# Performance work log

Hardware: AMD Instinct MI355X
Metric: run time of the kernel (lower is better)

## Reference

```python
import jax, jax.numpy as jnp
import numpy as np

TEMPERATURE = 0.1
B, D = 8192, 128
NUM_CLASSES = 100

def setup_inputs() -> dict:
    key = jax.random.key(0)
    k1, k2 = jax.random.split(key)
    embeddings = jax.random.normal(k1, (B, D), dtype=jnp.float32)
    labels = jax.random.randint(k2, (B,), 0, NUM_CLASSES, dtype=jnp.int64)
    return {"embeddings": embeddings, "labels": labels}

def reference(embeddings, labels):
    b = embeddings.shape[0]
    # L2-normalize rows (F.normalize with eps to avoid div-by-zero)
    norm = jnp.maximum(jnp.linalg.norm(embeddings, axis=1, keepdims=True), 1e-12)
    emb = embeddings / norm
    # [B, B] cosine similarities scaled by temperature
    sim = jnp.matmul(emb, emb.T) / TEMPERATURE
    eye = jnp.eye(b, dtype=jnp.float32)
    pos_mask = (labels[:, None] == labels[None, :]).astype(jnp.float32) - eye
    all_mask = 1.0 - eye
    # Original computes exp(sim*mask)*mask; since mask is {0,1}, this equals
    # exp(sim) summed over the masked entries.
    exp_sim = jnp.exp(sim)
    pos_sum = jnp.sum(exp_sim * pos_mask, axis=1)  # sum over positives j != i
    all_sum = jnp.sum(exp_sim * all_mask, axis=1)  # sum over all j != i
    valid = pos_sum > 0.0  # rows with no positives are skipped in the original
    pos_safe = jnp.where(valid, pos_sum, 1.0)
    all_safe = jnp.where(valid, all_sum, 1.0)
    row_loss = -jnp.log(pos_safe / all_safe)
    n_valid = jnp.sum(valid.astype(jnp.float32))
    loss = jnp.sum(jnp.where(valid, row_loss, 0.0)) / jnp.maximum(n_valid, 1.0)
    return loss
```

## Files before the change

kernel.cpp:

```cpp
#include <hip/hip_runtime.h>
#include <hip/hip_bf16.h>


#define B_ROWS 8192
#define D_DIM 128
#define K_SCALE 14.426950408889634f
#define JSPLIT 32
#define JCHUNK (B_ROWS / JSPLIT)
#define TILE_J 64
#define NT (JCHUNK / TILE_J)
#define BM 256

typedef __attribute__((ext_vector_type(8))) short bf16x8;
typedef __attribute__((ext_vector_type(16))) float f32x16;
typedef __attribute__((ext_vector_type(4))) unsigned int u32x4;
typedef unsigned int u32;
typedef unsigned long long u64;

static __device__ __forceinline__ unsigned short bf16_bits(float x) {
  __hip_bfloat16 h = __float2bfloat16(x);
  unsigned short u;
  __builtin_memcpy(&u, &h, 2);
  return u;
}
static __device__ __forceinline__ float f32_from_bits(u32 b) {
  float f;
  __builtin_memcpy(&f, &b, 4);
  return f;
}
static __device__ __forceinline__ float bf16f(unsigned short u) {
  return f32_from_bits((u32)u << 16);
}

__global__ __launch_bounds__(256) void prep_kernel(
    const float* __restrict__ E, const long long* __restrict__ labels,
    __hip_bfloat16* __restrict__ Ebf, __hip_bfloat16* __restrict__ Ebf2,
    int* __restrict__ lab32, unsigned char* __restrict__ lab8p,
    float* __restrict__ diag, u32* __restrict__ ticket) {
  if (blockIdx.x == 0 && threadIdx.x == 0) *ticket = 0u;
  const int wid = threadIdx.x >> 6, lane = threadIdx.x & 63;
  const int row = blockIdx.x * 4 + wid;
  const float2 v = *(const float2*)(E + (u64)row * D_DIM + lane * 2);
  float ss = v.x * v.x + v.y * v.y;
#pragma unroll
  for (int m = 1; m < 64; m <<= 1) ss += __shfl_xor(ss, m);
  const float scale = 1.0f / fmaxf(sqrtf(ss), 1e-12f);
  const unsigned short bx = bf16_bits(v.x * scale);
  const unsigned short by = bf16_bits(v.y * scale);
  ((u32*)Ebf)[(u64)row * (D_DIM / 2) + lane] = ((u32)by << 16) | bx;
  const float fx = bf16f(bx), fy = bf16f(by);
  const unsigned short axb = bf16_bits(fx * K_SCALE);
  const unsigned short ayb = bf16_bits(fy * K_SCALE);
  ((u32*)Ebf2)[(u64)row * (D_DIM / 2) + lane] = ((u32)ayb << 16) | axb;
  float dot = bf16f(axb) * fx + bf16f(ayb) * fy;
#pragma unroll
  for (int m = 1; m < 64; m <<= 1) dot += __shfl_xor(dot, m);
  if (lane == 0) diag[row] = __builtin_amdgcn_exp2f(dot);

  const int gtid = blockIdx.x * 256 + threadIdx.x;
  if (gtid < B_ROWS) {
    const int lab = (int)labels[gtid];
    lab32[gtid] = lab;
    const int local = gtid & 31;
    const int h = (local >> 2) & 1;
    const int r = (local & 3) + 4 * (local >> 3);
    lab8p[(gtid & ~31) + h * 16 + r] = (unsigned char)lab;
  }
}

__global__ __launch_bounds__(256, 3) void sim_kernel(
    const __hip_bfloat16* __restrict__ Ebf,
    const __hip_bfloat16* __restrict__ Ebf2, const int* __restrict__ lab32,
    const unsigned char* __restrict__ lab8p, float* __restrict__ pos_part,
    float* __restrict__ all_part) {
  __shared__ __align__(16) unsigned char lds[2][TILE_J * 256];

  const int t = threadIdx.x;
  const int wid = t >> 6, lane = t & 63;
  const int l31 = lane & 31, hi = lane >> 5;
  const int i0w = blockIdx.x * BM + wid * 64;
  const int jbase0 = blockIdx.y * JCHUNK;

  bf16x8 ifragA[8], ifragB[8];
  {
    const __hip_bfloat16* srcA = Ebf2 + (u64)(i0w + l31) * D_DIM + hi * 8;
    const __hip_bfloat16* srcB = srcA + 32 * D_DIM;
#pragma unroll
    for (int ks = 0; ks < 8; ++ks) {
      ifragA[ks] = *(const bf16x8*)(srcA + ks * 16);
      ifragB[ks] = *(const bf16x8*)(srcB + ks * 16);
    }
  }
  const int labi0 = lab32[i0w + l31];
  const int labi1 = lab32[i0w + 32 + l31];

  const u32 key = lane & 15;
  const u32 M = (key & 14) << 4;
  const u32 base2 = (u32)(l31 * 256) + (((hi ^ (key & 1)) & 1) << 4);

  const unsigned char* gsrc[4];
  {
    const unsigned char* gb = (const unsigned char*)Ebf;
    const int l4 = lane >> 4, sl = lane & 15;
#pragma unroll
    for (int i = 0; i < 4; ++i) {
      const int rloc = wid * 16 + i * 4 + l4;
      gsrc[i] =
          gb + (u64)(jbase0 + rloc) * 256 + (u64)((sl ^ (i * 4 + l4)) * 16);
    }
  }

  auto stage = [&](int buf) {
#pragma unroll
    for (int i = 0; i < 4; ++i) {
      __builtin_amdgcn_global_load_lds(
          (const __attribute__((address_space(1))) u32*)(gsrc[i]),
          (__attribute__((address_space(3)))
               u32*)(&lds[buf][wid * 4096 + i * 1024]),
          16, 0, 0);
      gsrc[i] += TILE_J * 256;
    }
  };

  float pos0 = 0.f, pos1 = 0.f, all0 = 0.f, all1 = 0.f;

  stage(0);
  __syncthreads();

  for (int tile = 0; tile < NT; ++tile) {
    const int cur = tile & 1;
    if (tile + 1 < NT) stage(cur ^ 1);
    const int jbase = jbase0 + tile * TILE_J;
    const unsigned char* lbuf = lds[cur];
#pragma unroll
    for (int jsub = 0; jsub < 2; ++jsub) {
      f32x16 acc0 = {}, acc1 = {};
#pragma unroll
      for (int ks = 0; ks < 8; ++ks) {
        bf16x8 jfrag = *(const bf16x8*)(lbuf + base2 +
                                        (((u32)(ks << 5)) ^ M) + jsub * 8192);
        acc0 = __builtin_amdgcn_mfma_f32_32x32x16_bf16(jfrag, ifragA[ks], acc0,
                                                       0, 0, 0);
        acc1 = __builtin_amdgcn_mfma_f32_32x32x16_bf16(jfrag, ifragB[ks], acc1,
                                                       0, 0, 0);
      }
      const u32x4 labv = *(const u32x4*)(lab8p + jbase + jsub * 32 + hi * 16);
#pragma unroll
      for (int r = 0; r < 16; ++r) {
        const int labj = (int)((labv[r >> 2] >> ((r & 3) * 8)) & 0xff);
        const float p0 = __builtin_amdgcn_exp2f(acc0[r]);
        const float p1 = __builtin_amdgcn_exp2f(acc1[r]);
        all0 += p0;
        all1 += p1;
        pos0 += (labj == labi0) ? p0 : 0.f;
        pos1 += (labj == labi1) ? p1 : 0.f;
      }
    }
    __syncthreads();
  }

  pos0 += __shfl_xor(pos0, 32);
  all0 += __shfl_xor(all0, 32);
  pos1 += __shfl_xor(pos1, 32);
  all1 += __shfl_xor(all1, 32);
  if (hi == 0) {
    const u64 off = (u64)blockIdx.y * B_ROWS;
    pos_part[off + i0w + l31] = pos0;
    all_part[off + i0w + l31] = all0;
    pos_part[off + i0w + 32 + l31] = pos1;
    all_part[off + i0w + 32 + l31] = all1;
  }
}

__global__ __launch_bounds__(256) void fin_kernel(
    const float* __restrict__ pos_part, const float* __restrict__ all_part,
    const float* __restrict__ diag, float* __restrict__ fin_s,
    float* __restrict__ fin_c, u32* __restrict__ ticket,
    float* __restrict__ out) {
  const int row = blockIdx.x * 256 + threadIdx.x;
  float ps = 0.f, as_ = 0.f;
#pragma unroll
  for (int js = 0; js < JSPLIT; ++js) {
    ps += pos_part[(u64)js * B_ROWS + row];
    as_ += all_part[(u64)js * B_ROWS + row];
  }
  const float d = diag[row];
  ps -= d;
  as_ -= d;
  float s = 0.f, c = 0.f;
  if (ps > 0.f) {
    s = logf(as_) - logf(ps);
    c = 1.f;
  }
#pragma unroll
  for (int m = 1; m < 64; m <<= 1) {
    s += __shfl_xor(s, m);
    c += __shfl_xor(c, m);
  }
  __shared__ float ls[4], lc[4];
  const int wid = threadIdx.x >> 6, lane = threadIdx.x & 63;
  if (lane == 0) {
    ls[wid] = s;
    lc[wid] = c;
  }
  __syncthreads();
  if (threadIdx.x == 0) {
    __hip_atomic_store(&fin_s[blockIdx.x], ls[0] + ls[1] + ls[2] + ls[3],
                       __ATOMIC_RELEASE, __HIP_MEMORY_SCOPE_AGENT);
    __hip_atomic_store(&fin_c[blockIdx.x], lc[0] + lc[1] + lc[2] + lc[3],
                       __ATOMIC_RELEASE, __HIP_MEMORY_SCOPE_AGENT);
    const u32 tk = __hip_atomic_fetch_add(ticket, 1u, __ATOMIC_ACQ_REL,
                                          __HIP_MEMORY_SCOPE_AGENT);
    if (tk == 31u) {
      float ts = 0.f, tc = 0.f;
      for (int b = 0; b < 32; ++b) {
        ts += __hip_atomic_load(&fin_s[b], __ATOMIC_ACQUIRE,
                                __HIP_MEMORY_SCOPE_AGENT);
        tc += __hip_atomic_load(&fin_c[b], __ATOMIC_ACQUIRE,
                                __HIP_MEMORY_SCOPE_AGENT);
      }
      out[0] = ts / fmaxf(tc, 1.0f);
    }
  }
}

extern "C" void kernel_launch(void* const* d_in, const int* in_sizes, int n_in,
                              void* d_out, int out_size, void* d_ws,
                              size_t ws_size, hipStream_t stream) {
  const float* E = (const float*)d_in[0];
  const long long* labels = (const long long*)d_in[1];

  float* pos_part = (float*)d_ws;
  float* all_part = pos_part + JSPLIT * B_ROWS;
  int* lab32 = (int*)(all_part + JSPLIT * B_ROWS);
  float* diag = (float*)(lab32 + B_ROWS);
  unsigned char* lab8p = (unsigned char*)(diag + B_ROWS);
  float* fin_s = (float*)(lab8p + B_ROWS);
  float* fin_c = fin_s + 32;
  u32* ticket = (u32*)(fin_c + 32);
  __hip_bfloat16* Ebf = (__hip_bfloat16*)(ticket + 4);
  __hip_bfloat16* Ebf2 = Ebf + (u64)B_ROWS * D_DIM;

  prep_kernel<<<B_ROWS / 4, 256, 0, stream>>>(E, labels, Ebf, Ebf2, lab32,
                                              lab8p, diag, ticket);
  sim_kernel<<<dim3(B_ROWS / BM, JSPLIT), 256, 0, stream>>>(
      Ebf, Ebf2, lab32, lab8p, pos_part, all_part);
  fin_kernel<<<JSPLIT, 256, 0, stream>>>(pos_part, all_part, diag, fin_s,
                                         fin_c, ticket, (float*)d_out);
}
```

Before: 53.28 us.

## Drop LDS staging in sim kernel, load j-fragments directly from global memory

The sim kernel no longer stages j-tiles into double-buffered LDS with global_load_lds and barriers. Each wave now loads its bf16 j-fragments straight from global memory (L2-cached) into registers before the MFMAs. JSPLIT doubles to 64 so each block handles 128 j rows, which gives twice as many blocks and removes the occupancy hint. This cuts LDS traffic and syncs, but every wave re-reads the same j data from cache, and the fin kernel now has to reduce twice as many partials.

```diff
diff --git a/kernel.cpp b/kernel.cpp
--- a/kernel.cpp
+++ b/kernel.cpp
@@ -5,10 +5,9 @@
 #define B_ROWS 8192
 #define D_DIM 128
 #define K_SCALE 14.426950408889634f
-#define JSPLIT 32
+#define JSPLIT 64
 #define JCHUNK (B_ROWS / JSPLIT)
-#define TILE_J 64
-#define NT (JCHUNK / TILE_J)
+#define NSUB (JCHUNK / 32)
 #define BM 256
 
 typedef __attribute__((ext_vector_type(8))) short bf16x8;
@@ -68,13 +67,11 @@
   }
 }
 
-__global__ __launch_bounds__(256, 3) void sim_kernel(
+__global__ __launch_bounds__(256) void sim_kernel(
     const __hip_bfloat16* __restrict__ Ebf,
     const __hip_bfloat16* __restrict__ Ebf2, const int* __restrict__ lab32,
     const unsigned char* __restrict__ lab8p, float* __restrict__ pos_part,
     float* __restrict__ all_part) {
-  __shared__ __align__(16) unsigned char lds[2][TILE_J * 256];
-
   const int t = threadIdx.x;
   const int wid = t >> 6, lane = t & 63;
   const int l31 = lane & 31, hi = lane >> 5;
@@ -94,69 +91,39 @@
   const int labi0 = lab32[i0w + l31];
   const int labi1 = lab32[i0w + 32 + l31];
 
-  const u32 key = lane & 15;
-  const u32 M = (key & 14) << 4;
-  const u32 base2 = (u32)(l31 * 256) + (((hi ^ (key & 1)) & 1) << 4);
-
-  const unsigned char* gsrc[4];
-  {
-    const unsigned char* gb = (const unsigned char*)Ebf;
-    const int l4 = lane >> 4, sl = lane & 15;
-#pragma unroll
-    for (int i = 0; i < 4; ++i) {
-      const int rloc = wid * 16 + i * 4 + l4;
-      gsrc[i] =
-          gb + (u64)(jbase0 + rloc) * 256 + (u64)((sl ^ (i * 4 + l4)) * 16);
-    }
-  }
-
-  auto stage = [&](int buf) {
-#pragma unroll
-    for (int i = 0; i < 4; ++i) {
-      __builtin_amdgcn_global_load_lds(
-          (const __attribute__((address_space(1))) u32*)(gsrc[i]),
-          (__attribute__((address_space(3)))
-               u32*)(&lds[buf][wid * 4096 + i * 1024]),
-          16, 0, 0);
-      gsrc[i] += TILE_J * 256;
-    }
-  };
+  const unsigned char* jsrc =
+      (const unsigned char*)Ebf + (u64)(jbase0 + l31) * 256 + hi * 16;
 
   float pos0 = 0.f, pos1 = 0.f, all0 = 0.f, all1 = 0.f;
 
-  stage(0);
-  __syncthreads();
-
-  for (int tile = 0; tile < NT; ++tile) {
-    const int cur = tile & 1;
-    if (tile + 1 < NT) stage(cur ^ 1);
-    const int jbase = jbase0 + tile * TILE_J;
-    const unsigned char* lbuf = lds[cur];
-#pragma unroll
-    for (int jsub = 0; jsub < 2; ++jsub) {
-      f32x16 acc0 = {}, acc1 = {};
-#pragma unroll
-      for (int ks = 0; ks < 8; ++ks) {
-        bf16x8 jfrag = *(const bf16x8*)(lbuf + base2 +
-                                        (((u32)(ks << 5)) ^ M) + jsub * 8192);
-        acc0 = __builtin_amdgcn_mfma_f32_32x32x16_bf16(jfrag, ifragA[ks], acc0,
-                                                       0, 0, 0);
-        acc1 = __builtin_amdgcn_mfma_f32_32x32x16_bf16(jfrag, ifragB[ks], acc1,
-                                                       0, 0, 0);
-      }
-      const u32x4 labv = *(const u32x4*)(lab8p + jbase + jsub * 32 + hi * 16);
-#pragma unroll
-      for (int r = 0; r < 16; ++r) {
-        const int labj = (int)((labv[r >> 2] >> ((r & 3) * 8)) & 0xff);
-        const float p0 = __builtin_amdgcn_exp2f(acc0[r]);
-        const float p1 = __builtin_amdgcn_exp2f(acc1[r]);
-        all0 += p0;
-        all1 += p1;
-        pos0 += (labj == labi0) ? p0 : 0.f;
-        pos1 += (labj == labi1) ? p1 : 0.f;
-      }
-    }
-    __syncthreads();
+#pragma unroll
+  for (int jsub = 0; jsub < NSUB; ++jsub) {
+    bf16x8 jf[8];
+#pragma unroll
+    for (int ks = 0; ks < 8; ++ks)
+      jf[ks] = *(const bf16x8*)(jsrc + (u64)jsub * (32 * 256) + ks * 32);
+
+    f32x16 acc0 = {}, acc1 = {};
+#pragma unroll
+    for (int ks = 0; ks < 8; ++ks) {
+      acc0 = __builtin_amdgcn_mfma_f32_32x32x16_bf16(jf[ks], ifragA[ks], acc0,
+                                                     0, 0, 0);
+      acc1 = __builtin_amdgcn_mfma_f32_32x32x16_bf16(jf[ks], ifragB[ks], acc1,
+                                                     0, 0, 0);
+    }
+
+    const u32x4 labv =
+        *(const u32x4*)(lab8p + jbase0 + jsub * 32 + hi * 16);
+#pragma unroll
+    for (int r = 0; r < 16; ++r) {
+      const int labj = (int)((labv[r >> 2] >> ((r & 3) * 8)) & 0xff);
+      const float p0 = __builtin_amdgcn_exp2f(acc0[r]);
+      const float p1 = __builtin_amdgcn_exp2f(acc1[r]);
+      all0 += p0;
+      all1 += p1;
+      pos0 += (labj == labi0) ? p0 : 0.f;
+      pos1 += (labj == labi1) ? p1 : 0.f;
+    }
   }
 
   pos0 += __shfl_xor(pos0, 32);
@@ -179,7 +146,7 @@
     float* __restrict__ out) {
   const int row = blockIdx.x * 256 + threadIdx.x;
   float ps = 0.f, as_ = 0.f;
-#pragma unroll
+#pragma unroll 8
   for (int js = 0; js < JSPLIT; ++js) {
     ps += pos_part[(u64)js * B_ROWS + row];
     as_ += all_part[(u64)js * B_ROWS + row];
@@ -245,6 +212,7 @@
                                               lab8p, diag, ticket);
   sim_kernel<<<dim3(B_ROWS / BM, JSPLIT), 256, 0, stream>>>(
       Ebf, Ebf2, lab32, lab8p, pos_part, all_part);
-  fin_kernel<<<JSPLIT, 256, 0, stream>>>(pos_part, all_part, diag, fin_s,
-                                         fin_c, ticket, (float*)d_out);
-}
+  fin_kernel<<<B_ROWS / 256, 256, 0, stream>>>(pos_part, all_part, diag,
+                                               fin_s, fin_c, ticket,
+                                               (float*)d_out);
+}
```

After: 73.03 us. 37.1% more time.
